# Kernel tuning notes

Measured on AMD Instinct MI355X. Metric: run time of the kernel, lower is better.

Reference implementation:

```python
import jax, jax.numpy as jnp
import numpy as np

B, L = 32, 512
D_EMB = 500      # tagger_mlp_layer
LANG = 100       # tagger_embeddings_size
H = 800          # tagger_encoder_size * 2
P_ARC = 100      # parser_arc_proj_size
P_LAB = 400      # parser_label_proj_size
MLP = 500        # tagger_mlp_layer (aux_mlp out)
N_LANG, N_LAB, N_UPOS, N_XPOS, N_ATTRS = 8, 50, 20, 300, 500


def setup_inputs() -> dict:
    key = jax.random.key(0)
    ks = jax.random.split(key, 24)
    s = 0.05
    lang_table = jax.random.normal(ks[3], (N_LANG, LANG), jnp.float32) * s
    lang_table = lang_table.at[0].set(0.0)  # padding_idx=0
    return {
        "emb": jax.random.normal(ks[0], (B, L, D_EMB), jnp.float32),
        "hidden": jax.random.normal(ks[1], (B, L, H), jnp.float32),
        "lang_ids": jax.random.randint(ks[2], (B,), 0, N_LANG),
        "lang_table": lang_table,
        "W_arc": jax.random.normal(ks[4], (P_ARC, D_EMB + LANG), jnp.float32) * s,
        "b_arc": jax.random.normal(ks[5], (P_ARC,), jnp.float32) * s,
        "W_lab": jax.random.normal(ks[6], (P_LAB, D_EMB + LANG), jnp.float32) * s,
        "b_lab": jax.random.normal(ks[7], (P_LAB,), jnp.float32) * s,
        "w_head": jax.random.normal(ks[8], (2 * P_ARC,), jnp.float32) * s,
        "b_head": jax.random.normal(ks[9], (1,), jnp.float32) * s,
        "W_aux": jax.random.normal(ks[10], (MLP, H), jnp.float32) * s,
        "b_aux": jax.random.normal(ks[11], (MLP,), jnp.float32) * s,
        "W_upos": jax.random.normal(ks[12], (N_UPOS, MLP + LANG), jnp.float32) * s,
        "b_upos": jax.random.normal(ks[13], (N_UPOS,), jnp.float32) * s,
        "W_xpos": jax.random.normal(ks[14], (N_XPOS, MLP + LANG), jnp.float32) * s,
        "b_xpos": jax.random.normal(ks[15], (N_XPOS,), jnp.float32) * s,
        "W_attrs": jax.random.normal(ks[16], (N_ATTRS, MLP + LANG), jnp.float32) * s,
        "b_attrs": jax.random.normal(ks[17], (N_ATTRS,), jnp.float32) * s,
    }


def reference(emb, hidden, lang_ids, lang_table, W_arc, b_arc, W_lab, b_lab,
              w_head, b_head, W_aux, b_aux, W_upos, b_upos, W_xpos, b_xpos,
              W_attrs, b_attrs):
    Bv, Lv = emb.shape[0], emb.shape[1]
    lang_emb = lang_table[lang_ids]                              # [B, LANG]
    lang_rep = jnp.broadcast_to(lang_emb[:, None, :], (Bv, Lv, lang_emb.shape[-1]))
    ho = jnp.concatenate((emb, lang_rep), axis=2)                # [B, L, D_EMB+LANG]

    proj_arc = jnp.tanh(jnp.einsum('bld,pd->blp', ho, W_arc) + b_arc)   # [B, L, P_ARC]
    proj_label = jnp.tanh(jnp.einsum('bld,pd->blp', ho, W_lab) + b_lab) # [B, L, P_LAB]

    # Biaffine decomposition of output_head(cat(pa[i], pa[j])):
    # score(i,j) = pa[i] . w1 + pa[j] . w2 + b
    P = proj_arc.shape[-1]
    s1 = proj_arc @ w_head[:P]                                   # [B, L]
    s2 = proj_arc @ w_head[P:]                                   # [B, L]
    core = s1[:, :, None] + s2[:, None, :] + b_head[0]           # [B, L, L]
    arcs = jnp.concatenate(
        (jnp.zeros((Bv, Lv, 1), core.dtype), core), axis=2)     # [B, L, L+1]

    aux_hid = jnp.tanh(jnp.einsum('blh,mh->blm', hidden, W_aux) + b_aux)  # [B, L, MLP]
    aux_cat = jnp.concatenate((aux_hid, lang_rep), axis=2)
    s_upos = jnp.einsum('blm,um->blu', aux_cat, W_upos) + b_upos
    s_xpos = jnp.einsum('blm,um->blu', aux_cat, W_xpos) + b_xpos
    s_attrs = jnp.einsum('blm,um->blu', aux_cat, W_attrs) + b_attrs
    return arcs, proj_label, s_upos, s_xpos, s_attrs
```

## Files before the change

kernel.cpp:

```cpp
#include <hip/hip_runtime.h>


using f16   = _Float16;
using f16x4 = __attribute__((ext_vector_type(4))) _Float16;
using f16x8 = __attribute__((ext_vector_type(8))) _Float16;
using f32x4 = __attribute__((ext_vector_type(4))) float;

__device__ __forceinline__ f16 f2h(float f) { return (f16)f; }
__device__ __forceinline__ f16x4 cvt4(float4 v) {
  return f16x4{ f2h(v.x), f2h(v.y), f2h(v.z), f2h(v.w) };
}

__device__ __forceinline__ float fast_tanh(float x) {
  float xc = fminf(fmaxf(x, -15.f), 15.f);
  float e  = __builtin_amdgcn_exp2f(xc * 2.885390081777927f);
  return 1.f - 2.f * __builtin_amdgcn_rcpf(e + 1.f);
}

__device__ __forceinline__ void async16(void* lds, const void* gp) {
  __builtin_amdgcn_global_load_lds(
      (const __attribute__((address_space(1))) unsigned int*)gp,
      (__attribute__((address_space(3))) unsigned int*)lds, 16, 0, 0);
}

__global__ __launch_bounds__(256) void setup_kernel(
    const float* __restrict__ W_arc, const float* __restrict__ b_arc,
    const float* __restrict__ W_lab, const float* __restrict__ b_lab,
    const float* __restrict__ W_aux, const float* __restrict__ b_aux,
    const float* __restrict__ W_upos, const float* __restrict__ b_upos,
    const float* __restrict__ W_xpos, const float* __restrict__ b_xpos,
    const float* __restrict__ W_attrs, const float* __restrict__ b_attrs,
    f16* __restrict__ W_proj, f16* __restrict__ W_auxp, f16* __restrict__ W_heads,
    float* __restrict__ bias_proj, float* __restrict__ bias_aux, float* __restrict__ bias_heads)
{
  const int blk = blockIdx.x, t = threadIdx.x;
  if (blk < 1376) {
    int w = blk * 256 + t;
    const float* src = nullptr;
    f16* dst;
    if (w < 81920) {
      int n = w / 160, s = w - n * 160;
      dst = W_proj + (size_t)w * 4;
      if (s < 150 && n < 500)
        src = (n < 100 ? W_arc + (size_t)n * 600
                       : W_lab + (size_t)(n - 100) * 600) + s * 4;
    } else if (w < 81920 + 106496) {
      int w2 = w - 81920;
      int n = w2 / 208, s = w2 - n * 208;
      dst = W_auxp + (size_t)w2 * 4;
      if (s < 200 && n < 500) src = W_aux + (size_t)n * 800 + s * 4;
    } else {
      int w3 = w - (81920 + 106496);
      int n = w3 / 160, s = w3 - n * 160;
      dst = W_heads + (size_t)w3 * 4;
      if (s < 150 && n < 820)
        src = (n < 20 ? W_upos + (size_t)n * 600
              : n < 320 ? W_xpos + (size_t)(n - 20) * 600
                        : W_attrs + (size_t)(n - 320) * 600) + s * 4;
    }
    f16x4 h = { (f16)0.f, (f16)0.f, (f16)0.f, (f16)0.f };
    if (src) h = cvt4(*(const float4*)src);
    *(f16x4*)dst = h;
    return;
  }
  for (int idx = t; idx < 2048; idx += 256) {
    if (idx < 512) {
      float v = 0.f;
      if (idx < 100)      v = b_arc[idx];
      else if (idx < 500) v = b_lab[idx - 100];
      bias_proj[idx] = v;
    } else if (idx < 1024) {
      int i = idx - 512;
      bias_aux[i] = (i < 500) ? b_aux[i] : 0.f;
    } else {
      int i = idx - 1024; float v = 0.f;
      if (i < 20)       v = b_upos[i];
      else if (i < 320) v = b_xpos[i - 20];
      else if (i < 820) v = b_attrs[i - 320];
      bias_heads[i] = v;
    }
  }
}

__global__ __launch_bounds__(512, 2) void gemm01(
    const float* __restrict__ emb, const float* __restrict__ hidden,
    const float* __restrict__ lang_table, const int* __restrict__ lang_ids,
    const f16* __restrict__ W_proj, const f16* __restrict__ W_auxp,
    const float* __restrict__ bias_proj, const float* __restrict__ bias_aux,
    float* __restrict__ out_label, const float* __restrict__ w_head,
    float* __restrict__ s1, float* __restrict__ s2, f16* __restrict__ aux_cat)
{
  __shared__ __align__(16) f16 ldsA[2 * 16384];
  __shared__ __align__(16) f16 ldsB[2 * 16384];
  __shared__ float s1red[2][256], s2red[2][256];

  const int tid  = threadIdx.x;
  const int lane = tid & 63;
  const int wave = tid >> 6;
  const int wm = wave >> 2, wn = wave & 3;
  const int m16 = lane & 15, quad = lane >> 4;
  const int bm  = blockIdx.x;
  const int bny = blockIdx.y;
  const bool is0 = (bny < 2);
  const int bn  = is0 ? bny : bny - 2;
  const int K   = is0 ? 640 : 832;
  const int NT  = is0 ? 10 : 13;

  const int sr = lane >> 3;
  const int ssB = (lane & 7) ^ sr;
  const f16* Bmat = is0 ? W_proj : W_auxp;
  const f16* gB[4];
#pragma unroll
  for (int i = 0; i < 4; ++i)
    gB[i] = Bmat + (size_t)(bn * 256 + i * 64 + wave * 8 + sr) * K + ssB * 8;
  f16* sB = ldsB + wave * 512;

  const int ssA = lane & 7;
  const float* lrow = lang_table + (size_t)lang_ids[bm >> 1] * 100;
  const float* srcA[4];
  int dstA[4];
#pragma unroll
  for (int i = 0; i < 4; ++i) {
    const int rowA = wave * 32 + i * 8 + (lane >> 3);
    const int grow = bm * 256 + rowA;
    srcA[i] = is0 ? emb + (size_t)grow * 500 : hidden + (size_t)grow * 800;
    dstA[i] = rowA * 64 + ((ssA ^ (rowA & 7)) * 8);
  }
  float4 va[4], vb[4];

  const int aBase = (wm * 128 + m16) * 64;
  const int bBase = (wn * 64  + m16) * 64;
  const int sw0 = ((quad)     ^ (m16 & 7)) * 8;
  const int sw1 = ((4 | quad) ^ (m16 & 7)) * 8;

  f32x4 acc[8][4] = {};
  f16x8 af[4], bf[4];

#define ASTAGE(tt) do { const int k0b = (tt) * 64 + ssA * 8;                    \
    _Pragma("unroll")                                                           \
    for (int i2 = 0; i2 < 4; ++i2) {                                            \
      float4 x0 = {0.f,0.f,0.f,0.f}, x1 = {0.f,0.f,0.f,0.f};                    \
      if (is0) {                                                                \
        if (k0b < 500) { x0 = *(const float4*)(srcA[i2] + k0b);                 \
          x1 = (k0b + 4 < 500) ? *(const float4*)(srcA[i2] + k0b + 4)           \
                               : *(const float4*)(lrow); }                      \
        else if (k0b < 600) { x0 = *(const float4*)(lrow + k0b - 500);          \
                              x1 = *(const float4*)(lrow + k0b - 496); }        \
      } else if (k0b < 800) { x0 = *(const float4*)(srcA[i2] + k0b);            \
                              x1 = *(const float4*)(srcA[i2] + k0b + 4); }      \
      va[i2] = x0; vb[i2] = x1; } } while (0)

#define AWRITE(nbf) do { _Pragma("unroll")                                      \
    for (int i2 = 0; i2 < 4; ++i2) {                                            \
      f16x8 hw = { f2h(va[i2].x), f2h(va[i2].y), f2h(va[i2].z), f2h(va[i2].w),  \
                   f2h(vb[i2].x), f2h(vb[i2].y), f2h(vb[i2].z), f2h(vb[i2].w) };\
      *(f16x8*)&ldsA[(nbf) + dstA[i2]] = hw; } } while (0)

#define RDA(mqv, sw) { _Pragma("unroll")                                        \
  for (int ii = 0; ii < 4; ++ii)                                                \
    af[ii] = *(const f16x8*)&ldsA[buf + aBase + (mqv) * 4096 + ii * 1024 + (sw)]; }
#define RDB(sw) { _Pragma("unroll")                                             \
  for (int j = 0; j < 4; ++j)                                                   \
    bf[j] = *(const f16x8*)&ldsB[buf + bBase + j * 1024 + (sw)]; }
#define MM(mqv) { _Pragma("unroll")                                             \
  for (int ii = 0; ii < 4; ++ii) { _Pragma("unroll")                            \
    for (int j = 0; j < 4; ++j)                                                 \
      acc[(mqv) * 4 + ii][j] = __builtin_amdgcn_mfma_f32_16x16x32_f16(          \
          af[ii], bf[j], acc[(mqv) * 4 + ii][j], 0, 0, 0); } }
#define VM0 { asm volatile("s_waitcnt vmcnt(0)" ::: "memory");                  \
              __builtin_amdgcn_sched_barrier(0); }
#define LGK0 { asm volatile("s_waitcnt lgkmcnt(0)" ::: "memory");               \
               __builtin_amdgcn_sched_barrier(0); }
#define BAR  __builtin_amdgcn_s_barrier()
#define PRIO1 __builtin_amdgcn_s_setprio(1)
#define PRIO0 __builtin_amdgcn_s_setprio(0)

#pragma unroll
  for (int i = 0; i < 4; ++i) async16(sB + i * 4096, gB[i]);
  ASTAGE(0);
  VM0;
  AWRITE(0);
  LGK0;
  BAR;

  for (int t = 0; t < NT; ++t) {
    const int buf = (t & 1) << 14;
    const int nbf = ((t + 1) & 1) << 14;
    const bool st = (t + 1 < NT);
    const int k0n = (t + 1) << 6;

    if (st) {
      async16(sB + nbf + 0 * 4096, gB[0] + k0n);
      async16(sB + nbf + 1 * 4096, gB[1] + k0n);
      async16(sB + nbf + 2 * 4096, gB[2] + k0n);
      async16(sB + nbf + 3 * 4096, gB[3] + k0n);
      ASTAGE(t + 1);
    }
    RDB(sw0); RDA(0, sw0);
    BAR;
    PRIO1; MM(0); PRIO0;
    BAR;
    RDA(1, sw0);
    BAR;
    PRIO1; MM(1); PRIO0;
    BAR;
    RDB(sw1); RDA(0, sw1);
    BAR;
    PRIO1; MM(0); PRIO0;
    BAR;
    RDA(1, sw1);
    if (st) { VM0; AWRITE(nbf); }
    LGK0;
    BAR;
    PRIO1; MM(1); PRIO0;
    BAR;
  }
#undef ASTAGE
#undef AWRITE
#undef RDA
#undef RDB
#undef MM
#undef VM0
#undef LGK0
#undef BAR
#undef PRIO1
#undef PRIO0

  const int row0 = bm * 256 + wm * 128 + quad * 4;
  const int colT = bn * 256 + wn * 64 + m16;

  if (is0) {
    const float* bias = bias_proj;
    float p1[8][4] = {}, p2[8][4] = {};
    const bool haveHead = (bn == 0);
#pragma unroll
    for (int ai = 0; ai < 8; ++ai) {
#pragma unroll
      for (int j = 0; j < 4; ++j) {
        const int col = colT + j * 16;
        const float bcol = bias[col];
        float w1c = 0.f, w2c = 0.f;
        if (haveHead && col < 100) { w1c = w_head[col]; w2c = w_head[100 + col]; }
#pragma unroll
        for (int r = 0; r < 4; ++r) {
          const int row = row0 + ai * 16 + r;
          float v = fast_tanh(acc[ai][j][r] + bcol);
          if (col >= 100 && col < 500) out_label[(size_t)row * 400 + col - 100] = v;
          p1[ai][r] += v * w1c;
          p2[ai][r] += v * w2c;
        }
      }
    }
    if (haveHead) {
      if (wn < 2) {
#pragma unroll
        for (int d = 1; d < 16; d <<= 1)
#pragma unroll
          for (int ai = 0; ai < 8; ++ai)
#pragma unroll
            for (int r = 0; r < 4; ++r) {
              p1[ai][r] += __shfl_xor(p1[ai][r], d);
              p2[ai][r] += __shfl_xor(p2[ai][r], d);
            }
        if (m16 == 0) {
#pragma unroll
          for (int ai = 0; ai < 8; ++ai)
#pragma unroll
            for (int r = 0; r < 4; ++r) {
              int rl = wm * 128 + ai * 16 + quad * 4 + r;
              s1red[wn][rl] = p1[ai][r];
              s2red[wn][rl] = p2[ai][r];
            }
        }
      }
      __syncthreads();
      if (tid < 256) s1[bm * 256 + tid] = s1red[0][tid] + s1red[1][tid];
      else { int t2 = tid - 256; s2[bm * 256 + t2] = s2red[0][t2] + s2red[1][t2]; }
    }
  } else {
    const float* bias = bias_aux;
#pragma unroll
    for (int ai = 0; ai < 8; ++ai)
#pragma unroll
      for (int j = 0; j < 4; ++j) {
        const int col = colT + j * 16;
        if (col < 500) {
          const float bcol = bias[col];
#pragma unroll
          for (int r = 0; r < 4; ++r) {
            const int row = row0 + ai * 16 + r;
            aux_cat[(size_t)row * 640 + col] = f2h(fast_tanh(acc[ai][j][r] + bcol));
          }
        }
      }
    if (bn == 0) {
      for (int idx = tid; idx < 256 * 35; idx += 512) {
        int rr = idx / 35, qq = idx - rr * 35;
        int col = 500 + 4 * qq;
        f16x4 h = { (f16)0.f, (f16)0.f, (f16)0.f, (f16)0.f };
        if (col < 600) h = cvt4(*(const float4*)(lrow + col - 500));
        *(f16x4*)(aux_cat + (size_t)(bm * 256 + rr) * 640 + col) = h;
      }
    }
  }
}

__global__ __launch_bounds__(512, 2) void gemm2_arcs(
    const f16* __restrict__ aux_cat, const f16* __restrict__ W_heads,
    const float* __restrict__ bias_heads,
    const float* __restrict__ s1, const float* __restrict__ s2,
    const float* __restrict__ b_head,
    float* __restrict__ out_arcs, float* __restrict__ out_upos,
    float* __restrict__ out_xpos, float* __restrict__ out_attrs)
{
  __shared__ __align__(16) f16 ldsA[2 * 16384];
  __shared__ __align__(16) f16 ldsB[2 * 16384];

  const int tid  = threadIdx.x;
  const int lane = tid & 63;
  const int wave = tid >> 6;
  const int wm = wave >> 2, wn = wave & 3;
  const int m16 = lane & 15, quad = lane >> 4;
  const int bm = blockIdx.x, bn = blockIdx.y;
  const int K = 640, NT = 10;

  const int sr = lane >> 3;
  const int ss = (lane & 7) ^ sr;
  const f16* gA[4]; const f16* gB[4];
#pragma unroll
  for (int i = 0; i < 4; ++i) {
    gA[i] = aux_cat + (size_t)(bm * 256 + i * 64 + wave * 8 + sr) * K + ss * 8;
    gB[i] = W_heads + (size_t)(bn * 256 + i * 64 + wave * 8 + sr) * K + ss * 8;
  }
  f16* sA = ldsA + wave * 512;
  f16* sB = ldsB + wave * 512;

  const int aBase = (wm * 128 + m16) * 64;
  const int bBase = (wn * 64  + m16) * 64;
  const int sw0 = ((quad)     ^ (m16 & 7)) * 8;
  const int sw1 = ((4 | quad) ^ (m16 & 7)) * 8;

  f32x4 acc[8][4] = {};
  f16x8 af[4], bf[4];

#define RDA(mqv, sw) { _Pragma("unroll")                                        \
  for (int ii = 0; ii < 4; ++ii)                                                \
    af[ii] = *(const f16x8*)&ldsA[buf + aBase + (mqv) * 4096 + ii * 1024 + (sw)]; }
#define RDB(sw) { _Pragma("unroll")                                             \
  for (int j = 0; j < 4; ++j)                                                   \
    bf[j] = *(const f16x8*)&ldsB[buf + bBase + j * 1024 + (sw)]; }
#define MM(mqv) { _Pragma("unroll")                                             \
  for (int ii = 0; ii < 4; ++ii) { _Pragma("unroll")                            \
    for (int j = 0; j < 4; ++j)                                                 \
      acc[(mqv) * 4 + ii][j] = __builtin_amdgcn_mfma_f32_16x16x32_f16(          \
          af[ii], bf[j], acc[(mqv) * 4 + ii][j], 0, 0, 0); } }
#define VM2 { asm volatile("s_waitcnt vmcnt(2)" ::: "memory");                  \
              __builtin_amdgcn_sched_barrier(0); }
#define VM0 { asm volatile("s_waitcnt vmcnt(0)" ::: "memory");                  \
              __builtin_amdgcn_sched_barrier(0); }
#define BAR  __builtin_amdgcn_s_barrier()
#define PRIO1 __builtin_amdgcn_s_setprio(1)
#define PRIO0 __builtin_amdgcn_s_setprio(0)

#pragma unroll
  for (int i = 0; i < 4; ++i) async16(sB + i * 4096, gB[i]);
#pragma unroll
  for (int i = 0; i < 4; ++i) async16(sA + i * 4096, gA[i]);
  VM0;
  BAR;

  for (int t = 0; t < NT; ++t) {
    const int buf = (t & 1) << 14;
    const int nbf = ((t + 1) & 1) << 14;
    const bool st = (t + 1 < NT);
    const int k0n = (t + 1) << 6;

    if (st) { async16(sB + nbf + 0 * 4096, gB[0] + k0n);
              async16(sB + nbf + 1 * 4096, gB[1] + k0n); }
    RDB(sw0); RDA(0, sw0);
    BAR;
    PRIO1; MM(0); PRIO0;
    if (t > 0) { if (st) VM2 else VM0 }
    BAR;
    if (st) { async16(sB + nbf + 2 * 4096, gB[2] + k0n);
              async16(sB + nbf + 3 * 4096, gB[3] + k0n); }
    RDA(1, sw0);
    BAR;
    PRIO1; MM(1); PRIO0;
    BAR;
    if (st) { async16(sA + nbf + 0 * 4096, gA[0] + k0n);
              async16(sA + nbf + 2 * 4096, gA[2] + k0n); }
    RDB(sw1); RDA(0, sw1);
    BAR;
    PRIO1; MM(0); PRIO0;
    BAR;
    if (st) { async16(sA + nbf + 1 * 4096, gA[1] + k0n);
              async16(sA + nbf + 3 * 4096, gA[3] + k0n); }
    RDA(1, sw1);
    BAR;
    PRIO1; MM(1); PRIO0;
    if (st) VM2;
    BAR;
  }
#undef RDA
#undef RDB
#undef MM
#undef VM2
#undef VM0
#undef BAR
#undef PRIO1
#undef PRIO0

  const int row0 = bm * 256 + wm * 128 + quad * 4;
  const int colT = bn * 256 + wn * 64 + m16;
#pragma unroll
  for (int ai = 0; ai < 8; ++ai)
#pragma unroll
    for (int j = 0; j < 4; ++j) {
      const int col = colT + j * 16;
      const float bcol = bias_heads[col];
#pragma unroll
      for (int r = 0; r < 4; ++r) {
        const int row = row0 + ai * 16 + r;
        float v = acc[ai][j][r] + bcol;
        if (col < 20)        out_upos[(size_t)row * 20 + col] = v;
        else if (col < 320)  out_xpos[(size_t)row * 300 + col - 20] = v;
        else if (col < 820)  out_attrs[(size_t)row * 500 + col - 320] = v;
      }
    }

  const int r0 = bm * 256 + bn * 64;
  const float bh = b_head[0];
  const float s2v = s2[((r0 >> 9) << 9) + tid];
  for (int rl = 0; rl < 64; ++rl) {
    const int row = r0 + rl;
    const float s1v = s1[row] + bh;
    float* orow = out_arcs + (size_t)row * 513;
    if (tid == 0) orow[0] = 0.f;
    orow[1 + tid] = s1v + s2v;
  }
}

extern "C" void kernel_launch(void* const* d_in, const int* in_sizes, int n_in,
                              void* d_out, int out_size, void* d_ws, size_t ws_size,
                              hipStream_t stream)
{
  const float* emb      = (const float*)d_in[0];
  const float* hidden   = (const float*)d_in[1];
  const int*   lang_ids = (const int*)d_in[2];
  const float* lang_tab = (const float*)d_in[3];
  const float* W_arc  = (const float*)d_in[4];
  const float* b_arc  = (const float*)d_in[5];
  const float* W_lab  = (const float*)d_in[6];
  const float* b_lab  = (const float*)d_in[7];
  const float* w_head = (const float*)d_in[8];
  const float* b_head = (const float*)d_in[9];
  const float* W_aux  = (const float*)d_in[10];
  const float* b_aux  = (const float*)d_in[11];
  const float* W_upos = (const float*)d_in[12];
  const float* b_upos = (const float*)d_in[13];
  const float* W_xpos = (const float*)d_in[14];
  const float* b_xpos = (const float*)d_in[15];
  const float* W_attrs = (const float*)d_in[16];
  const float* b_attrs = (const float*)d_in[17];

  char* ws = (char*)d_ws;
  f16* aux_cat = (f16*)(ws + 0);
  f16* W_proj  = (f16*)(ws + 20971520);
  f16* W_auxp  = (f16*)(ws + 21626880);
  f16* W_heads = (f16*)(ws + 22478848);
  float* bias_proj  = (float*)(ws + 23789568);
  float* bias_aux   = (float*)(ws + 23791616);
  float* bias_heads = (float*)(ws + 23793664);
  float* s1         = (float*)(ws + 23797760);
  float* s2         = (float*)(ws + 23863296);

  float* out       = (float*)d_out;
  float* out_arcs  = out;
  float* out_label = out + 8404992;
  float* out_upos  = out + 14958592;
  float* out_xpos  = out + 15286272;
  float* out_attrs = out + 20201472;

  setup_kernel<<<1377, 256, 0, stream>>>(
      W_arc, b_arc, W_lab, b_lab, W_aux, b_aux,
      W_upos, b_upos, W_xpos, b_xpos, W_attrs, b_attrs,
      W_proj, W_auxp, W_heads, bias_proj, bias_aux, bias_heads);

  gemm01<<<dim3(64, 4), 512, 0, stream>>>(
      emb, hidden, lang_tab, lang_ids, W_proj, W_auxp, bias_proj, bias_aux,
      out_label, w_head, s1, s2, aux_cat);

  gemm2_arcs<<<dim3(64, 4), 512, 0, stream>>>(
      aux_cat, W_heads, bias_heads, s1, s2, b_head,
      out_arcs, out_upos, out_xpos, out_attrs);
}
```

Measured before the change: 283.4 us.

## Collapse per-phase barriers into single end-of-iteration barrier in both GEMM loops

Both MFMA main loops drop the many intermediate s_barriers between LDS-read and MFMA phases. Each loop now issues all next-tile global-to-LDS loads right after the first fragment reads, and ends with one wait-then-barrier per K step. The sched_barrier fences are also removed from the waitcnt macros. The aim is to cut barrier stalls and let the compiler interleave work, at the cost of less staggered load issue and possible LDS pressure from waves drifting apart.

```diff
diff --git a/kernel.cpp b/kernel.cpp
--- a/kernel.cpp
+++ b/kernel.cpp
@@ -156,6 +156,12 @@
                    f2h(vb[i2].x), f2h(vb[i2].y), f2h(vb[i2].z), f2h(vb[i2].w) };\
       *(f16x8*)&ldsA[(nbf) + dstA[i2]] = hw; } } while (0)
 
+#define BWISSUE(k0n, nbf) do {                                                  \
+    async16(sB + (nbf) + 0 * 4096, gB[0] + (k0n));                              \
+    async16(sB + (nbf) + 1 * 4096, gB[1] + (k0n));                              \
+    async16(sB + (nbf) + 2 * 4096, gB[2] + (k0n));                              \
+    async16(sB + (nbf) + 3 * 4096, gB[3] + (k0n)); } while (0)
+
 #define RDA(mqv, sw) { _Pragma("unroll")                                        \
   for (int ii = 0; ii < 4; ++ii)                                                \
     af[ii] = *(const f16x8*)&ldsA[buf + aBase + (mqv) * 4096 + ii * 1024 + (sw)]; }
@@ -167,19 +173,16 @@
     for (int j = 0; j < 4; ++j)                                                 \
       acc[(mqv) * 4 + ii][j] = __builtin_amdgcn_mfma_f32_16x16x32_f16(          \
           af[ii], bf[j], acc[(mqv) * 4 + ii][j], 0, 0, 0); } }
-#define VM0 { asm volatile("s_waitcnt vmcnt(0)" ::: "memory");                  \
-              __builtin_amdgcn_sched_barrier(0); }
-#define LGK0 { asm volatile("s_waitcnt lgkmcnt(0)" ::: "memory");               \
-               __builtin_amdgcn_sched_barrier(0); }
+#define VM0  asm volatile("s_waitcnt vmcnt(0)" ::: "memory")
+#define LGK0 asm volatile("s_waitcnt lgkmcnt(0)" ::: "memory")
 #define BAR  __builtin_amdgcn_s_barrier()
 #define PRIO1 __builtin_amdgcn_s_setprio(1)
 #define PRIO0 __builtin_amdgcn_s_setprio(0)
 
-#pragma unroll
-  for (int i = 0; i < 4; ++i) async16(sB + i * 4096, gB[i]);
   ASTAGE(0);
+  BWISSUE(0, 0);
+  AWRITE(0);
   VM0;
-  AWRITE(0);
   LGK0;
   BAR;
 
@@ -189,34 +192,23 @@
     const bool st = (t + 1 < NT);
     const int k0n = (t + 1) << 6;
 
-    if (st) {
-      async16(sB + nbf + 0 * 4096, gB[0] + k0n);
-      async16(sB + nbf + 1 * 4096, gB[1] + k0n);
-      async16(sB + nbf + 2 * 4096, gB[2] + k0n);
-      async16(sB + nbf + 3 * 4096, gB[3] + k0n);
-      ASTAGE(t + 1);
-    }
     RDB(sw0); RDA(0, sw0);
-    BAR;
+    if (st) { ASTAGE(t + 1); BWISSUE(k0n, nbf); }
     PRIO1; MM(0); PRIO0;
-    BAR;
     RDA(1, sw0);
-    BAR;
     PRIO1; MM(1); PRIO0;
-    BAR;
     RDB(sw1); RDA(0, sw1);
-    BAR;
     PRIO1; MM(0); PRIO0;
-    BAR;
     RDA(1, sw1);
-    if (st) { VM0; AWRITE(nbf); }
+    PRIO1; MM(1); PRIO0;
+    if (st) AWRITE(nbf);
+    VM0;
     LGK0;
     BAR;
-    PRIO1; MM(1); PRIO0;
-    BAR;
   }
 #undef ASTAGE
 #undef AWRITE
+#undef BWISSUE
 #undef RDA
 #undef RDB
 #undef MM
@@ -343,6 +335,16 @@
   f32x4 acc[8][4] = {};
   f16x8 af[4], bf[4];
 
+#define STAGE8(k0n, nbf) do {                                                   \
+    async16(sA + (nbf) + 0 * 4096, gA[0] + (k0n));                              \
+    async16(sA + (nbf) + 1 * 4096, gA[1] + (k0n));                              \
+    async16(sA + (nbf) + 2 * 4096, gA[2] + (k0n));                              \
+    async16(sA + (nbf) + 3 * 4096, gA[3] + (k0n));                              \
+    async16(sB + (nbf) + 0 * 4096, gB[0] + (k0n));                              \
+    async16(sB + (nbf) + 1 * 4096, gB[1] + (k0n));                              \
+    async16(sB + (nbf) + 2 * 4096, gB[2] + (k0n));                              \
+    async16(sB + (nbf) + 3 * 4096, gB[3] + (k0n)); } while (0)
+
 #define RDA(mqv, sw) { _Pragma("unroll")                                        \
   for (int ii = 0; ii < 4; ++ii)                                                \
     af[ii] = *(const f16x8*)&ldsA[buf + aBase + (mqv) * 4096 + ii * 1024 + (sw)]; }
@@ -354,18 +356,12 @@
     for (int j = 0; j < 4; ++j)                                                 \
       acc[(mqv) * 4 + ii][j] = __builtin_amdgcn_mfma_f32_16x16x32_f16(          \
           af[ii], bf[j], acc[(mqv) * 4 + ii][j], 0, 0, 0); } }
-#define VM2 { asm volatile("s_waitcnt vmcnt(2)" ::: "memory");                  \
-              __builtin_amdgcn_sched_barrier(0); }
-#define VM0 { asm volatile("s_waitcnt vmcnt(0)" ::: "memory");                  \
-              __builtin_amdgcn_sched_barrier(0); }
+#define VM0  asm volatile("s_waitcnt vmcnt(0)" ::: "memory")
 #define BAR  __builtin_amdgcn_s_barrier()
 #define PRIO1 __builtin_amdgcn_s_setprio(1)
 #define PRIO0 __builtin_amdgcn_s_setprio(0)
 
-#pragma unroll
-  for (int i = 0; i < 4; ++i) async16(sB + i * 4096, gB[i]);
-#pragma unroll
-  for (int i = 0; i < 4; ++i) async16(sA + i * 4096, gA[i]);
+  STAGE8(0, 0);
   VM0;
   BAR;
 
@@ -375,37 +371,22 @@
     const bool st = (t + 1 < NT);
     const int k0n = (t + 1) << 6;
 
-    if (st) { async16(sB + nbf + 0 * 4096, gB[0] + k0n);
-              async16(sB + nbf + 1 * 4096, gB[1] + k0n); }
     RDB(sw0); RDA(0, sw0);
+    if (st) STAGE8(k0n, nbf);
+    PRIO1; MM(0); PRIO0;
+    RDA(1, sw0);
+    PRIO1; MM(1); PRIO0;
+    RDB(sw1); RDA(0, sw1);
+    PRIO1; MM(0); PRIO0;
+    RDA(1, sw1);
+    PRIO1; MM(1); PRIO0;
+    VM0;
     BAR;
-    PRIO1; MM(0); PRIO0;
-    if (t > 0) { if (st) VM2 else VM0 }
-    BAR;
-    if (st) { async16(sB + nbf + 2 * 4096, gB[2] + k0n);
-              async16(sB + nbf + 3 * 4096, gB[3] + k0n); }
-    RDA(1, sw0);
-    BAR;
-    PRIO1; MM(1); PRIO0;
-    BAR;
-    if (st) { async16(sA + nbf + 0 * 4096, gA[0] + k0n);
-              async16(sA + nbf + 2 * 4096, gA[2] + k0n); }
-    RDB(sw1); RDA(0, sw1);
-    BAR;
-    PRIO1; MM(0); PRIO0;
-    BAR;
-    if (st) { async16(sA + nbf + 1 * 4096, gA[1] + k0n);
-              async16(sA + nbf + 3 * 4096, gA[3] + k0n); }
-    RDA(1, sw1);
-    BAR;
-    PRIO1; MM(1); PRIO0;
-    if (st) VM2;
-    BAR;
-  }
+  }
+#undef STAGE8
 #undef RDA
 #undef RDB
 #undef MM
-#undef VM2
 #undef VM0
 #undef BAR
 #undef PRIO1
```

Result: faster. 274.3 us (-3.2%).
